# Kernel optimization log

Measured on AMD Instinct MI355X. Metric: run time of the kernel, lower is better.

Reference implementation:

```python
import jax, jax.numpy as jnp
import numpy as np

MARGIN = 0.3
BATCH = 4096
FEAT = 256
NUM_IDS = 512


def setup_inputs() -> dict:
    key = jax.random.key(0)
    k1, k2 = jax.random.split(key)
    features = jax.random.normal(k1, (BATCH, FEAT), dtype=jnp.float32)
    labels = jax.random.randint(k2, (BATCH,), 0, NUM_IDS, dtype=jnp.int64 if jax.config.jax_enable_x64 else jnp.int32)
    return {"features": features, "labels": labels}


def reference(features, labels):
    n = features.shape[0]
    sq_norm = jnp.sum(features * features, axis=-1)  # [n]
    sq = sq_norm[:, None] + sq_norm[None, :] - 2.0 * (features @ features.T)
    dist = jnp.sqrt(jnp.maximum(sq, 1e-12))  # [n, n], == torch.cdist p=2

    same = labels[:, None] == labels[None, :]           # [n, n]
    eye = jnp.eye(n, dtype=bool)
    pos_mask = same & ~eye
    neg_mask = ~same

    NEG_INF = jnp.float32(-1e30)
    POS_INF = jnp.float32(1e30)
    hard_pos = jnp.max(jnp.where(pos_mask, dist, NEG_INF), axis=1)  # [n]
    hard_neg = jnp.min(jnp.where(neg_mask, dist, POS_INF), axis=1)  # [n]

    valid = pos_mask.any(axis=1) & neg_mask.any(axis=1)
    row_loss = jnp.maximum(hard_pos - hard_neg + MARGIN, 0.0)
    count = jnp.sum(valid)
    total = jnp.sum(jnp.where(valid, row_loss, 0.0))
    return jnp.where(count > 0, total / jnp.maximum(count, 1).astype(total.dtype), jnp.float32(0.0))
```

## Files before the change

kernel.cpp:

```cpp
#include <hip/hip_runtime.h>

typedef unsigned short ushort_t;
typedef __attribute__((ext_vector_type(8))) short bf16x8;
typedef __attribute__((ext_vector_type(4))) float f32x4;

#define NROWS 4096
#define DIM   256
#define NT    32
#define MARGINF 0.3f

__device__ __forceinline__ unsigned enc_f(float f) {
  unsigned u = __float_as_uint(f);
  return (u & 0x80000000u) ? ~u : (u | 0x80000000u);
}
__device__ __forceinline__ float dec_f(unsigned k) {
  unsigned u = (k & 0x80000000u) ? (k ^ 0x80000000u) : ~k;
  return __uint_as_float(u);
}

__device__ __forceinline__ ushort_t f2b(float f) {
  unsigned u = __float_as_uint(f);
  u += 0x7fffu + ((u >> 16) & 1u);
  return (ushort_t)(u >> 16);
}

__device__ __forceinline__ void gload_lds16(const void* g, void* l) {
  __builtin_amdgcn_global_load_lds(
      (const __attribute__((address_space(1))) void*)g,
      (__attribute__((address_space(3))) void*)l, 16, 0, 0);
}

__global__ void k_prep(const float* __restrict__ F, ushort_t* __restrict__ Fb,
                       float* __restrict__ nrm, unsigned* __restrict__ posk,
                       unsigned* __restrict__ negk) {
  const int tid = threadIdx.x;
  const int wave = tid >> 6, lane = tid & 63;
  const int row = blockIdx.x * 4 + wave;

  const float4 v = *(const float4*)&F[row * DIM + lane * 4];
  float s = fmaf(v.x, v.x, fmaf(v.y, v.y, fmaf(v.z, v.z, v.w * v.w)));
  #pragma unroll
  for (int off = 32; off; off >>= 1) s += __shfl_down(s, off);
  if (lane == 0) nrm[row] = s;

  ushort4 o;
  o.x = f2b(v.x); o.y = f2b(v.y); o.z = f2b(v.z); o.w = f2b(v.w);
  *(ushort4*)&Fb[row * DIM + lane * 4] = o;

  const int gid = blockIdx.x * 256 + tid;
  if (gid < NROWS) { posk[gid] = enc_f(-1e30f); negk[gid] = enc_f(1e30f); }
}

__global__ __launch_bounds__(256, 3) void k_gram(
    const ushort_t* __restrict__ Fb, const int* __restrict__ lab,
    const float* __restrict__ nrm,
    unsigned* __restrict__ posk, unsigned* __restrict__ negk) {
  __shared__ alignas(16) ushort_t As[2][128 * 32];
  __shared__ alignas(16) ushort_t Bs[2][128 * 32];
  __shared__ int labi[128], labj[128];
  __shared__ float nrmi[128], nrmj[128];
  __shared__ float redp[2][128], redn[2][128];
  __shared__ float redpc[2][128], rednc[2][128];

  const int tid = threadIdx.x;
  const int wave = tid >> 6, lane = tid & 63;
  const int wm = wave >> 1, wn = wave & 1;

  int rem = blockIdx.x, rt = 0;
  while (rem >= NT - rt) { rem -= NT - rt; ++rt; }
  const int ct = rt + rem;
  const int row0 = rt * 128, col0 = ct * 128;
  const bool isdiag = (rt == ct);

  if (tid < 128) { labi[tid] = lab[row0 + tid]; nrmi[tid] = nrm[row0 + tid]; }
  else { int t = tid - 128; labj[t] = lab[col0 + t]; nrmj[t] = nrm[col0 + t]; }

  f32x4 acc[4][4];
  #pragma unroll
  for (int m = 0; m < 4; ++m)
    #pragma unroll
    for (int n = 0; n < 4; ++n) acc[m][n] = (f32x4){0.f, 0.f, 0.f, 0.f};

  const int lrow = lane >> 2;
  const int lcol = (lane & 3) * 8;

  #pragma unroll
  for (int s = 0; s < 2; ++s) {
    const int rbase = s * 64 + wave * 16;
    gload_lds16(&Fb[(row0 + rbase + lrow) * DIM + lcol], &As[0][rbase * 32]);
    gload_lds16(&Fb[(col0 + rbase + lrow) * DIM + lcol], &Bs[0][rbase * 32]);
  }
  __syncthreads();

  for (int kk = 0; kk < 8; ++kk) {
    const int cur = kk & 1;
    if (kk < 7) {
      const int nxt = cur ^ 1;
      #pragma unroll
      for (int s = 0; s < 2; ++s) {
        const int rbase = s * 64 + wave * 16;
        gload_lds16(&Fb[(row0 + rbase + lrow) * DIM + (kk + 1) * 32 + lcol], &As[nxt][rbase * 32]);
        gload_lds16(&Fb[(col0 + rbase + lrow) * DIM + (kk + 1) * 32 + lcol], &Bs[nxt][rbase * 32]);
      }
    }
    bf16x8 a[4], b[4];
    #pragma unroll
    for (int m = 0; m < 4; ++m)
      a[m] = *(const bf16x8*)&As[cur][(wm * 64 + m * 16 + (lane & 15)) * 32 + (lane >> 4) * 8];
    #pragma unroll
    for (int n = 0; n < 4; ++n)
      b[n] = *(const bf16x8*)&Bs[cur][(wn * 64 + n * 16 + (lane & 15)) * 32 + (lane >> 4) * 8];
    #pragma unroll
    for (int m = 0; m < 4; ++m)
      #pragma unroll
      for (int n = 0; n < 4; ++n)
        acc[m][n] = __builtin_amdgcn_mfma_f32_16x16x32_bf16(a[m], b[n], acc[m][n], 0, 0, 0);
    __syncthreads();
  }

  const int h = lane >> 4, ccol = lane & 15;
  float posr[4][4], negr[4][4];
  float posc[4], negc[4];
  #pragma unroll
  for (int m = 0; m < 4; ++m)
    #pragma unroll
    for (int j = 0; j < 4; ++j) { posr[m][j] = -1e30f; negr[m][j] = 1e30f; }
  #pragma unroll
  for (int n = 0; n < 4; ++n) { posc[n] = -1e30f; negc[n] = 1e30f; }

  #pragma unroll
  for (int m = 0; m < 4; ++m) {
    #pragma unroll
    for (int n = 0; n < 4; ++n) {
      const int cl = wn * 64 + n * 16 + ccol;
      const float nj = nrmj[cl];
      const int lj = labj[cl];
      #pragma unroll
      for (int j = 0; j < 4; ++j) {
        const int rl = wm * 64 + m * 16 + h * 4 + j;
        const float sq = nrmi[rl] + nj - 2.f * acc[m][n][j];
        const bool same = (labi[rl] == lj);
        const bool self = isdiag && (rl == cl);
        if (same) {
          if (!self) {
            posr[m][j] = fmaxf(posr[m][j], sq);
            posc[n] = fmaxf(posc[n], sq);
          }
        } else {
          negr[m][j] = fminf(negr[m][j], sq);
          negc[n] = fminf(negc[n], sq);
        }
      }
    }
  }

  #pragma unroll
  for (int m = 0; m < 4; ++m) {
    #pragma unroll
    for (int j = 0; j < 4; ++j) {
      float p = posr[m][j], q = negr[m][j];
      #pragma unroll
      for (int mask = 1; mask <= 8; mask <<= 1) {
        p = fmaxf(p, __shfl_xor(p, mask));
        q = fminf(q, __shfl_xor(q, mask));
      }
      if (ccol == 0) {
        const int rl = wm * 64 + m * 16 + h * 4 + j;
        redp[wn][rl] = p; redn[wn][rl] = q;
      }
    }
  }
  #pragma unroll
  for (int n = 0; n < 4; ++n) {
    float p = posc[n], q = negc[n];
    #pragma unroll
    for (int mask = 16; mask <= 32; mask <<= 1) {
      p = fmaxf(p, __shfl_xor(p, mask));
      q = fminf(q, __shfl_xor(q, mask));
    }
    if (lane < 16) {
      redpc[wm][wn * 64 + n * 16 + lane] = p;
      rednc[wm][wn * 64 + n * 16 + lane] = q;
    }
  }
  __syncthreads();

  if (tid < 128) {
    const float p = fmaxf(redp[0][tid], redp[1][tid]);
    const float q = fminf(redn[0][tid], redn[1][tid]);
    atomicMax(&posk[row0 + tid], enc_f(p));
    atomicMin(&negk[row0 + tid], enc_f(q));
    if (!isdiag) {
      const float pc = fmaxf(redpc[0][tid], redpc[1][tid]);
      const float qc = fminf(rednc[0][tid], rednc[1][tid]);
      atomicMax(&posk[col0 + tid], enc_f(pc));
      atomicMin(&negk[col0 + tid], enc_f(qc));
    }
  }
}

__global__ void k_final(const unsigned* __restrict__ posk,
                        const unsigned* __restrict__ negk,
                        float* __restrict__ out) {
  int t = threadIdx.x;
  float sum = 0.f;
  int cnt = 0;
  for (int i = t; i < NROWS; i += 1024) {
    float ps = dec_f(posk[i]);
    float ns = dec_f(negk[i]);
    if ((ps > -1e29f) && (ns < 1e29f)) {
      float hp = sqrtf(fmaxf(ps, 1e-12f));
      float hn = sqrtf(fmaxf(ns, 1e-12f));
      sum += fmaxf(hp - hn + MARGINF, 0.f);
      cnt += 1;
    }
  }
  #pragma unroll
  for (int off = 32; off; off >>= 1) {
    sum += __shfl_down(sum, off);
    cnt += __shfl_down(cnt, off);
  }
  __shared__ float wsum[16];
  __shared__ int wcnt[16];
  int w = t >> 6;
  if ((t & 63) == 0) { wsum[w] = sum; wcnt[w] = cnt; }
  __syncthreads();
  if (t == 0) {
    float S = 0.f; int C = 0;
    #pragma unroll
    for (int i = 0; i < 16; ++i) { S += wsum[i]; C += wcnt[i]; }
    out[0] = (C > 0) ? (S / (float)C) : 0.f;
  }
}

extern "C" void kernel_launch(void* const* d_in, const int* in_sizes, int n_in,
                              void* d_out, int out_size, void* d_ws, size_t ws_size,
                              hipStream_t stream) {
  const float* F = (const float*)d_in[0];
  const int* lab = (const int*)d_in[1];
  float* out = (float*)d_out;

  unsigned* posk = (unsigned*)d_ws;
  unsigned* negk = posk + NROWS;
  float* nrm = (float*)(negk + NROWS);
  ushort_t* Fb = (ushort_t*)(nrm + NROWS);

  k_prep<<<NROWS / 4, 256, 0, stream>>>(F, Fb, nrm, posk, negk);
  k_gram<<<NT * (NT + 1) / 2, 256, 0, stream>>>(Fb, lab, nrm, posk, negk);
  k_final<<<1, 1024, 0, stream>>>(posk, negk, out);
}
```

Before: 80.05 us.

## Pre-swizzle bf16 features into MFMA fragment layout and load directly from global

The prep kernel now writes the bf16 features in a blocked layout where each 16-row by 8-column MFMA fragment is contiguous. The gram kernel drops its LDS double-buffered staging and its per-iteration barriers, loading operand fragments straight from global memory into registers with coalesced 16-byte loads. This removes LDS traffic and synchronisation, but operand reuse across waves now comes only from L1/L2, and the fully unrolled loop may raise register pressure.

```diff
diff --git a/kernel.cpp b/kernel.cpp
--- a/kernel.cpp
+++ b/kernel.cpp
@@ -7,6 +7,7 @@
 #define NROWS 4096
 #define DIM   256
 #define NT    32
+#define NBLK  (NT * (NT + 1) / 2)
 #define MARGINF 0.3f
 
 __device__ __forceinline__ unsigned enc_f(float f) {
@@ -24,13 +25,8 @@
   return (ushort_t)(u >> 16);
 }
 
-__device__ __forceinline__ void gload_lds16(const void* g, void* l) {
-  __builtin_amdgcn_global_load_lds(
-      (const __attribute__((address_space(1))) void*)g,
-      (__attribute__((address_space(3))) void*)l, 16, 0, 0);
-}
-
-__global__ void k_prep(const float* __restrict__ F, ushort_t* __restrict__ Fb,
+
+__global__ void k_prep(const float* __restrict__ F, ushort_t* __restrict__ Fb2,
                        float* __restrict__ nrm, unsigned* __restrict__ posk,
                        unsigned* __restrict__ negk) {
   const int tid = threadIdx.x;
@@ -45,18 +41,19 @@
 
   ushort4 o;
   o.x = f2b(v.x); o.y = f2b(v.y); o.z = f2b(v.z); o.w = f2b(v.w);
-  *(ushort4*)&Fb[row * DIM + lane * 4] = o;
+  const int k0 = lane * 4;
+  const unsigned idx = (unsigned)(row >> 4) * 4096u + (unsigned)(k0 >> 3) * 128u
+                     + (unsigned)(row & 15) * 8u + (unsigned)(k0 & 7);
+  *(ushort4*)&Fb2[idx] = o;
 
   const int gid = blockIdx.x * 256 + tid;
   if (gid < NROWS) { posk[gid] = enc_f(-1e30f); negk[gid] = enc_f(1e30f); }
 }
 
 __global__ __launch_bounds__(256, 3) void k_gram(
-    const ushort_t* __restrict__ Fb, const int* __restrict__ lab,
+    const ushort_t* __restrict__ Fb2, const int* __restrict__ lab,
     const float* __restrict__ nrm,
     unsigned* __restrict__ posk, unsigned* __restrict__ negk) {
-  __shared__ alignas(16) ushort_t As[2][128 * 32];
-  __shared__ alignas(16) ushort_t Bs[2][128 * 32];
   __shared__ int labi[128], labj[128];
   __shared__ float nrmi[128], nrmj[128];
   __shared__ float redp[2][128], redn[2][128];
@@ -74,6 +71,12 @@
 
   if (tid < 128) { labi[tid] = lab[row0 + tid]; nrmi[tid] = nrm[row0 + tid]; }
   else { int t = tid - 128; labj[t] = lab[col0 + t]; nrmj[t] = nrm[col0 + t]; }
+  __syncthreads();
+
+  const int h = lane >> 4, r = lane & 15;
+  const unsigned fbase = (unsigned)h * 128u + (unsigned)r * 8u;
+  const unsigned abase = (unsigned)(rt * 8 + wm * 4) * 4096u + fbase;
+  const unsigned bbase = (unsigned)(ct * 8 + wn * 4) * 4096u + fbase;
 
   f32x4 acc[4][4];
   #pragma unroll
@@ -81,44 +84,23 @@
     #pragma unroll
     for (int n = 0; n < 4; ++n) acc[m][n] = (f32x4){0.f, 0.f, 0.f, 0.f};
 
-  const int lrow = lane >> 2;
-  const int lcol = (lane & 3) * 8;
-
-  #pragma unroll
-  for (int s = 0; s < 2; ++s) {
-    const int rbase = s * 64 + wave * 16;
-    gload_lds16(&Fb[(row0 + rbase + lrow) * DIM + lcol], &As[0][rbase * 32]);
-    gload_lds16(&Fb[(col0 + rbase + lrow) * DIM + lcol], &Bs[0][rbase * 32]);
-  }
-  __syncthreads();
-
+  #pragma unroll
   for (int kk = 0; kk < 8; ++kk) {
-    const int cur = kk & 1;
-    if (kk < 7) {
-      const int nxt = cur ^ 1;
-      #pragma unroll
-      for (int s = 0; s < 2; ++s) {
-        const int rbase = s * 64 + wave * 16;
-        gload_lds16(&Fb[(row0 + rbase + lrow) * DIM + (kk + 1) * 32 + lcol], &As[nxt][rbase * 32]);
-        gload_lds16(&Fb[(col0 + rbase + lrow) * DIM + (kk + 1) * 32 + lcol], &Bs[nxt][rbase * 32]);
-      }
-    }
     bf16x8 a[4], b[4];
     #pragma unroll
     for (int m = 0; m < 4; ++m)
-      a[m] = *(const bf16x8*)&As[cur][(wm * 64 + m * 16 + (lane & 15)) * 32 + (lane >> 4) * 8];
+      a[m] = *(const bf16x8*)&Fb2[abase + (unsigned)m * 4096u + (unsigned)kk * 512u];
     #pragma unroll
     for (int n = 0; n < 4; ++n)
-      b[n] = *(const bf16x8*)&Bs[cur][(wn * 64 + n * 16 + (lane & 15)) * 32 + (lane >> 4) * 8];
+      b[n] = *(const bf16x8*)&Fb2[bbase + (unsigned)n * 4096u + (unsigned)kk * 512u];
     #pragma unroll
     for (int m = 0; m < 4; ++m)
       #pragma unroll
       for (int n = 0; n < 4; ++n)
         acc[m][n] = __builtin_amdgcn_mfma_f32_16x16x32_bf16(a[m], b[n], acc[m][n], 0, 0, 0);
-    __syncthreads();
-  }
-
-  const int h = lane >> 4, ccol = lane & 15;
+  }
+
+  const int ccol = r;
   float posr[4][4], negr[4][4];
   float posc[4], negc[4];
   #pragma unroll
@@ -243,9 +225,9 @@
   unsigned* posk = (unsigned*)d_ws;
   unsigned* negk = posk + NROWS;
   float* nrm = (float*)(negk + NROWS);
-  ushort_t* Fb = (ushort_t*)(nrm + NROWS);
-
-  k_prep<<<NROWS / 4, 256, 0, stream>>>(F, Fb, nrm, posk, negk);
-  k_gram<<<NT * (NT + 1) / 2, 256, 0, stream>>>(Fb, lab, nrm, posk, negk);
+  ushort_t* Fb2 = (ushort_t*)(nrm + NROWS);
+
+  k_prep<<<NROWS / 4, 256, 0, stream>>>(F, Fb2, nrm, posk, negk);
+  k_gram<<<NBLK, 256, 0, stream>>>(Fb2, lab, nrm, posk, negk);
   k_final<<<1, 1024, 0, stream>>>(posk, negk, out);
 }
```

Result: no change. 78.78 us (median of 2 runs) (-1.6%).
